# Kernel optimization log

Hardware: AMD Instinct MI355X
Metric: run time of the kernel (lower is better)

Reference implementation:

```python
import jax, jax.numpy as jnp
import numpy as np

N_HEAD = 16


def setup_inputs() -> dict:
    key = jax.random.key(0)
    ks = jax.random.split(key, 5)
    B, T, D_IN, D = 2, 2048, 1152, 1024
    s_in = 1.0 / np.sqrt(D_IN)
    s_d = 1.0 / np.sqrt(D)
    return {
        "xp": jax.random.normal(ks[0], (B, T, D_IN), jnp.float32),
        "Wq": jax.random.normal(ks[1], (D_IN, D), jnp.float32) * s_in,
        "bq": jnp.zeros((D,), jnp.float32),
        "Wk": jax.random.normal(ks[2], (D_IN, D), jnp.float32) * s_in,
        "bk": jnp.zeros((D,), jnp.float32),
        "Wv": jax.random.normal(ks[3], (D_IN, D), jnp.float32) * s_in,
        "bv": jnp.zeros((D,), jnp.float32),
        "Wp": jax.random.normal(ks[4], (D, D), jnp.float32) * s_d,
        "bp": jnp.zeros((D,), jnp.float32),
    }


def reference(xp, Wq, bq, Wk, bk, Wv, bv, Wp, bp):
    B, T, _ = xp.shape
    D = Wq.shape[1]
    hd = D // N_HEAD  # head dim
    # q, k, v projections -> [B, H, T, hd]
    def split_heads(t):
        return t.reshape(B, T, N_HEAD, hd).transpose(0, 2, 1, 3)
    q = split_heads(xp @ Wq + bq)
    k = split_heads(xp @ Wk + bk)
    v = split_heads(xp @ Wv + bv)
    scale = 1.0 / np.sqrt(hd).astype(np.float32)
    att = jnp.einsum("bhqd,bhkd->bhqk", q, k) * scale  # [B,H,T,T]
    causal = jnp.tril(jnp.ones((T, T), bool))
    att = jnp.where(causal[None, None], att, -jnp.inf)
    att = jax.nn.softmax(att, axis=-1)
    y = jnp.einsum("bhqk,bhkd->bhqd", att, v)  # [B,H,T,hd]
    y = y.transpose(0, 2, 1, 3).reshape(B, T, D)
    return y @ Wp + bp
```

## Files before the change

### kernel.cpp

```cpp
#include <hip/hip_runtime.h>
#include <hip/hip_bf16.h>

typedef __attribute__((ext_vector_type(8))) short bf16x8;
typedef __attribute__((ext_vector_type(4))) short bf16x4;
typedef __attribute__((ext_vector_type(4))) float f32x4;

__device__ __forceinline__ void gload_lds16(const void* g, void* l) {
    __builtin_amdgcn_global_load_lds(
        (const __attribute__((address_space(1))) unsigned int*)g,
        (__attribute__((address_space(3))) unsigned int*)l, 16, 0, 0);
}

__device__ __forceinline__ f32x4 mfma_16x16x16(bf16x4 a, bf16x4 b, f32x4 c) {
#if __has_builtin(__builtin_amdgcn_mfma_f32_16x16x16bf16_1k)
    return __builtin_amdgcn_mfma_f32_16x16x16bf16_1k(a, b, c, 0, 0, 0);
#else
    f32x4 d = c;
    asm volatile("v_mfma_f32_16x16x16_bf16 %0, %1, %2, %0" : "+v"(d) : "v"(a), "v"(b));
    return d;
#endif
}

__global__ void k_cvt_bf16(const float* __restrict__ x, __hip_bfloat16* __restrict__ o, int n8) {
    int i = blockIdx.x * 256 + threadIdx.x;
    if (i >= n8) return;
    const float4* xp = (const float4*)(x + (size_t)i * 8);
    float4 a = xp[0], b = xp[1];
    union { __hip_bfloat16 h[8]; uint4 u; } tu;
    tu.h[0] = __float2bfloat16(a.x); tu.h[1] = __float2bfloat16(a.y);
    tu.h[2] = __float2bfloat16(a.z); tu.h[3] = __float2bfloat16(a.w);
    tu.h[4] = __float2bfloat16(b.x); tu.h[5] = __float2bfloat16(b.y);
    tu.h[6] = __float2bfloat16(b.z); tu.h[7] = __float2bfloat16(b.w);
    *(uint4*)(o + (size_t)i * 8) = tu.u;
}

__global__ void k_tr3(const float* __restrict__ s0, const float* __restrict__ s1,
                      const float* __restrict__ s2, __hip_bfloat16* __restrict__ dst,
                      int K, int N) {
    __shared__ float tile[32][33];
    const float* src = (blockIdx.z == 0) ? s0 : ((blockIdx.z == 1) ? s1 : s2);
    __hip_bfloat16* d = dst + (size_t)blockIdx.z * N * K;
    int n0 = blockIdx.x * 32, k0 = blockIdx.y * 32;
    int tx = threadIdx.x & 31, ty = threadIdx.x >> 5;
#pragma unroll
    for (int i = 0; i < 4; i++)
        tile[ty + i * 8][tx] = src[(size_t)(k0 + ty + i * 8) * N + n0 + tx];
    __syncthreads();
#pragma unroll
    for (int i = 0; i < 4; i++)
        d[(size_t)(n0 + ty + i * 8) * K + k0 + tx] = __float2bfloat16(tile[tx][ty + i * 8]);
}

__global__ void k_tr(const float* __restrict__ src, __hip_bfloat16* __restrict__ dst, int K, int N) {
    __shared__ float tile[32][33];
    int n0 = blockIdx.x * 32, k0 = blockIdx.y * 32;
    int tx = threadIdx.x & 31, ty = threadIdx.x >> 5;
#pragma unroll
    for (int i = 0; i < 4; i++)
        tile[ty + i * 8][tx] = src[(size_t)(k0 + ty + i * 8) * N + n0 + tx];
    __syncthreads();
#pragma unroll
    for (int i = 0; i < 4; i++)
        dst[(size_t)(n0 + ty + i * 8) * K + k0 + tx] = __float2bfloat16(tile[tx][ty + i * 8]);
}

#define QSCALE 0.18033688011111204f

template <int EPI>
__global__ __launch_bounds__(256, 2) void k_gemm(
    const __hip_bfloat16* __restrict__ A, const __hip_bfloat16* __restrict__ Bt,
    int M, int N, int K,
    const float* __restrict__ b0, const float* __restrict__ b1, const float* __restrict__ b2,
    __hip_bfloat16* __restrict__ qb, __hip_bfloat16* __restrict__ kb, __hip_bfloat16* __restrict__ vb,
    float* __restrict__ outp, int mtiles)
{
    __shared__ __align__(16) __hip_bfloat16 As[128 * 64];
    __shared__ __align__(16) __hip_bfloat16 Bs[128 * 64];
    const int t = threadIdx.x;
    const int lane = t & 63, w = t >> 6;
    const int wr = w >> 1, wc = w & 1;
    const int r16 = lane & 15, kg = lane >> 4;
    const int cpx = gridDim.x >> 3;
    const int bid = blockIdx.x;
    const int swz = (bid & 7) * cpx + (bid >> 3);
    const int m0 = (swz % mtiles) * 128, n0 = (swz / mtiles) * 128;
    f32x4 acc[4][4] = {};
    const int ksteps = K >> 6;
    for (int kt = 0; kt < ksteps; ++kt) {
        if (kt) __syncthreads();
        const int ks = kt * 64;
#pragma unroll
        for (int i = 0; i < 4; i++) {
            int ci = i * 256 + t;
            int row = ci >> 3, kc = (ci & 7) * 8;
            gload_lds16(A + (size_t)(m0 + row) * K + ks + kc, As + ci * 8);
        }
#pragma unroll
        for (int i = 0; i < 4; i++) {
            int ci = i * 256 + t;
            int row = ci >> 3, kc = (ci & 7) * 8;
            gload_lds16(Bt + (size_t)(n0 + row) * K + ks + kc, Bs + ci * 8);
        }
        __syncthreads();
#pragma unroll
        for (int c = 0; c < 2; c++) {
            bf16x8 af[4], bfr[4];
#pragma unroll
            for (int mi = 0; mi < 4; mi++)
                af[mi] = *(const bf16x8*)(As + (wr * 64 + mi * 16 + r16) * 64 + c * 32 + kg * 8);
#pragma unroll
            for (int ni = 0; ni < 4; ni++)
                bfr[ni] = *(const bf16x8*)(Bs + (wc * 64 + ni * 16 + r16) * 64 + c * 32 + kg * 8);
#pragma unroll
            for (int mi = 0; mi < 4; mi++)
#pragma unroll
                for (int ni = 0; ni < 4; ni++)
                    acc[mi][ni] = __builtin_amdgcn_mfma_f32_16x16x32_bf16(af[mi], bfr[ni], acc[mi][ni], 0, 0, 0);
        }
    }
#pragma unroll
    for (int mi = 0; mi < 4; mi++) {
#pragma unroll
        for (int ni = 0; ni < 4; ni++) {
#pragma unroll
            for (int j = 0; j < 4; j++) {
                int m = m0 + wr * 64 + mi * 16 + kg * 4 + j;
                int n = n0 + wc * 64 + ni * 16 + r16;
                float val = acc[mi][ni][j];
                if (EPI == 0) {
                    int proj = n >> 10, r = n & 1023;
                    int hh = r >> 6, dd = r & 63;
                    int bb = m >> 11, tt = m & 2047;
                    if (proj == 0) {
                        val = (val + b0[r]) * QSCALE;
                        qb[((size_t)(bb * 16 + hh) * 2048 + tt) * 64 + dd] = __float2bfloat16(val);
                    } else if (proj == 1) {
                        val += b1[r];
                        kb[((size_t)(bb * 16 + hh) * 2048 + tt) * 64 + dd] = __float2bfloat16(val);
                    } else {
                        val += b2[r];
                        vb[((size_t)(bb * 16 + hh) * 64 + dd) * 2048 + tt] = __float2bfloat16(val);
                    }
                } else {
                    outp[(size_t)m * N + n] = val + b0[n];
                }
            }
        }
    }
}

__global__ __launch_bounds__(256, 4) void k_attn(
    const __hip_bfloat16* __restrict__ qbuf,
    const __hip_bfloat16* __restrict__ kbuf,
    const __hip_bfloat16* __restrict__ vtbuf,
    __hip_bfloat16* __restrict__ y)
{
    __shared__ __align__(16) __hip_bfloat16 Kl[2][64 * 64];
    __shared__ __align__(16) __hip_bfloat16 Vl[2][64 * 64];
    const int t = threadIdx.x, lane = t & 63, w = t >> 6;
    const int r16 = lane & 15, kg = lane >> 4;
    const int g = blockIdx.x;
    const int c4 = g >> 8, p = g & 255;
    const int bh = (p >> 5) * 4 + c4;
    const int rr = p & 31;
    const int qt = (c4 & 1) ? rr : 31 - rr;
    const int swr = (r16 & 7) << 3;
    const int q0 = qt * 64 + w * 16;
    const __hip_bfloat16* qp = qbuf + ((size_t)bh * 2048 + q0) * 64;
    bf16x8 qf0 = *(const bf16x8*)(qp + r16 * 64 + kg * 8);
    bf16x8 qf1 = *(const bf16x8*)(qp + r16 * 64 + 32 + kg * 8);
    f32x4 O[4] = {};
    float m_s = -3.0e38f, l_s = 0.f;
    const __hip_bfloat16* kb = kbuf + (size_t)bh * 2048 * 64;
    const __hip_bfloat16* vb = vtbuf + (size_t)bh * 64 * 2048;

    const int ci0 = t, ci1 = 256 + t;
    const int kr0 = ci0 >> 3, sc0 = ((ci0 & 7) * 8) ^ ((kr0 & 7) << 3);
    const int kr1 = ci1 >> 3, sc1 = ((ci1 & 7) * 8) ^ ((kr1 & 7) << 3);

    gload_lds16(kb + (size_t)kr0 * 64 + sc0, &Kl[0][ci0 * 8]);
    gload_lds16(kb + (size_t)kr1 * 64 + sc1, &Kl[0][ci1 * 8]);
    gload_lds16(vb + (size_t)kr0 * 2048 + sc0, &Vl[0][ci0 * 8]);
    gload_lds16(vb + (size_t)kr1 * 2048 + sc1, &Vl[0][ci1 * 8]);
    __syncthreads();

    for (int kt = 0; kt <= qt; ++kt) {
        const int cur = kt & 1;
        if (kt < qt) {
            const int kn = kt + 1;
            gload_lds16(kb + (size_t)kn * 4096 + (size_t)kr0 * 64 + sc0, &Kl[cur ^ 1][ci0 * 8]);
            gload_lds16(kb + (size_t)kn * 4096 + (size_t)kr1 * 64 + sc1, &Kl[cur ^ 1][ci1 * 8]);
            gload_lds16(vb + (size_t)kr0 * 2048 + kn * 64 + sc0, &Vl[cur ^ 1][ci0 * 8]);
            gload_lds16(vb + (size_t)kr1 * 2048 + kn * 64 + sc1, &Vl[cur ^ 1][ci1 * 8]);
        }
        const int kbase = kt * 64;
        if (kbase <= q0 + 15) {
            const __hip_bfloat16* Klb = Kl[cur];
            const __hip_bfloat16* Vlb = Vl[cur];
            f32x4 S[4];
            __builtin_amdgcn_s_setprio(1);
#pragma unroll
            for (int ct = 0; ct < 4; ct++) {
                f32x4 s = {};
                const int r = ct * 16 + r16;
                bf16x8 kf0 = *(const bf16x8*)(Klb + r * 64 + ((kg * 8) ^ swr));
                s = __builtin_amdgcn_mfma_f32_16x16x32_bf16(kf0, qf0, s, 0, 0, 0);
                bf16x8 kf1 = *(const bf16x8*)(Klb + r * 64 + ((32 + kg * 8) ^ swr));
                s = __builtin_amdgcn_mfma_f32_16x16x32_bf16(kf1, qf1, s, 0, 0, 0);
                S[ct] = s;
            }
            __builtin_amdgcn_s_setprio(0);
            if (kbase + 63 > q0) {
#pragma unroll
                for (int ct = 0; ct < 4; ct++)
#pragma unroll
                    for (int j = 0; j < 4; j++)
                        if (kbase + ct * 16 + kg * 4 + j > q0 + r16) S[ct][j] = -3.0e38f;
            }
            float rmax = S[0][0];
#pragma unroll
            for (int ct = 0; ct < 4; ct++)
#pragma unroll
                for (int j = 0; j < 4; j++) rmax = fmaxf(rmax, S[ct][j]);
            rmax = fmaxf(rmax, __shfl_xor(rmax, 16));
            rmax = fmaxf(rmax, __shfl_xor(rmax, 32));
            if (__any(rmax > m_s + 8.0f)) {
                const float mn = fmaxf(m_s, rmax);
                const float al = exp2f(m_s - mn);
                m_s = mn;
                l_s *= al;
#pragma unroll
                for (int j = 0; j < 4; j++) {
                    const float aj = __shfl(al, kg * 4 + j);
#pragma unroll
                    for (int ot = 0; ot < 4; ot++) O[ot][j] *= aj;
                }
            }
            float rsum = 0.f;
#pragma unroll
            for (int ct = 0; ct < 4; ct++)
#pragma unroll
                for (int j = 0; j < 4; j++) { S[ct][j] = exp2f(S[ct][j] - m_s); rsum += S[ct][j]; }
            rsum += __shfl_xor(rsum, 16);
            rsum += __shfl_xor(rsum, 32);
            l_s += rsum;
            bf16x4 pa[4];
#pragma unroll
            for (int ct = 0; ct < 4; ct++) {
                union { __hip_bfloat16 h[4]; bf16x4 v; } pk;
                pk.h[0] = __float2bfloat16(S[ct][0]);
                pk.h[1] = __float2bfloat16(S[ct][1]);
                pk.h[2] = __float2bfloat16(S[ct][2]);
                pk.h[3] = __float2bfloat16(S[ct][3]);
                pa[ct] = pk.v;
            }
            __builtin_amdgcn_s_setprio(1);
#pragma unroll
            for (int ot = 0; ot < 4; ot++) {
                const int vrow = ot * 16 + r16;
#pragma unroll
                for (int ct = 0; ct < 4; ct++) {
                    bf16x4 vf = *(const bf16x4*)(Vlb + vrow * 64 + ((ct * 16 + kg * 4) ^ ((vrow & 7) << 3)));
                    O[ot] = mfma_16x16x16(pa[ct], vf, O[ot]);
                }
            }
            __builtin_amdgcn_s_setprio(0);
        }
        __syncthreads();
    }
    const int b = bh >> 4, h = bh & 15;
    const float linv = 1.0f / l_s;
#pragma unroll
    for (int j = 0; j < 4; j++) {
        const float iv = __shfl(linv, kg * 4 + j);
        const int qq = q0 + kg * 4 + j;
#pragma unroll
        for (int ot = 0; ot < 4; ot++)
            y[((size_t)b * 2048 + qq) * 1024 + h * 64 + ot * 16 + r16] = __float2bfloat16(O[ot][j] * iv);
    }
}

extern "C" void kernel_launch(void* const* d_in, const int* in_sizes, int n_in,
                              void* d_out, int out_size, void* d_ws, size_t ws_size,
                              hipStream_t stream) {
    const float* xp = (const float*)d_in[0];
    const float* Wq = (const float*)d_in[1];
    const float* bq = (const float*)d_in[2];
    const float* Wk = (const float*)d_in[3];
    const float* bk = (const float*)d_in[4];
    const float* Wv = (const float*)d_in[5];
    const float* bv = (const float*)d_in[6];
    const float* Wp = (const float*)d_in[7];
    const float* bp = (const float*)d_in[8];
    float* out = (float*)d_out;

    char* ws = (char*)d_ws;
    __hip_bfloat16* xb     = (__hip_bfloat16*)(ws);
    __hip_bfloat16* Wqkv_t = (__hip_bfloat16*)(ws + 9437184);
    __hip_bfloat16* Wp_t   = (__hip_bfloat16*)(ws + 16515072);
    __hip_bfloat16* qb     = (__hip_bfloat16*)(ws + 18612224);
    __hip_bfloat16* kbv    = (__hip_bfloat16*)(ws + 27000832);
    __hip_bfloat16* vtb    = (__hip_bfloat16*)(ws + 35389440);
    __hip_bfloat16* yb     = (__hip_bfloat16*)(ws + 43778048);

    k_cvt_bf16<<<2304, 256, 0, stream>>>(xp, xb, 589824);
    dim3 trg3(1024 / 32, 1152 / 32, 3);
    k_tr3<<<trg3, 256, 0, stream>>>(Wq, Wk, Wv, Wqkv_t, 1152, 1024);
    dim3 trg2(1024 / 32, 1024 / 32);
    k_tr<<<trg2, 256, 0, stream>>>(Wp, Wp_t, 1024, 1024);

    k_gemm<0><<<768, 256, 0, stream>>>(xb, Wqkv_t, 4096, 3072, 1152, bq, bk, bv, qb, kbv, vtb,
                                       nullptr, 32);
    k_attn<<<1024, 256, 0, stream>>>(qb, kbv, vtb, yb);
    k_gemm<1><<<256, 256, 0, stream>>>(yb, Wp_t, 4096, 1024, 1024, bp, nullptr, nullptr,
                                       nullptr, nullptr, nullptr, out, 32);
}
```

Before: 157.2 us.

## Widen attention KV tile to 128 and use plain 2D GEMM grid

The attention kernel now stages 128 keys and values per iteration instead of 64, with 64 KB of double-buffered LDS, and processes eight score column tiles per step. This halves the number of loop iterations and barriers per block. In exchange it allows fewer resident blocks per CU (launch bound 4 to 2), raises register pressure, and does wasted masked work on the diagonal tile, which is now twice as wide. Separately, the GEMMs drop their XCD-aware block swizzle in favour of a plain 2D grid, which may change L2 locality.

Measured after the change: 159.1 us. About the same (+1.3%).

```diff
diff --git a/kernel.cpp b/kernel.cpp
--- a/kernel.cpp
+++ b/kernel.cpp
@@ -72,7 +72,7 @@
     int M, int N, int K,
     const float* __restrict__ b0, const float* __restrict__ b1, const float* __restrict__ b2,
     __hip_bfloat16* __restrict__ qb, __hip_bfloat16* __restrict__ kb, __hip_bfloat16* __restrict__ vb,
-    float* __restrict__ outp, int mtiles)
+    float* __restrict__ outp)
 {
     __shared__ __align__(16) __hip_bfloat16 As[128 * 64];
     __shared__ __align__(16) __hip_bfloat16 Bs[128 * 64];
@@ -80,10 +80,7 @@
     const int lane = t & 63, w = t >> 6;
     const int wr = w >> 1, wc = w & 1;
     const int r16 = lane & 15, kg = lane >> 4;
-    const int cpx = gridDim.x >> 3;
-    const int bid = blockIdx.x;
-    const int swz = (bid & 7) * cpx + (bid >> 3);
-    const int m0 = (swz % mtiles) * 128, n0 = (swz / mtiles) * 128;
+    const int m0 = blockIdx.x * 128, n0 = blockIdx.y * 128;
     f32x4 acc[4][4] = {};
     const int ksteps = K >> 6;
     for (int kt = 0; kt < ksteps; ++kt) {
@@ -149,14 +146,14 @@
     }
 }
 
-__global__ __launch_bounds__(256, 4) void k_attn(
+__global__ __launch_bounds__(256, 2) void k_attn(
     const __hip_bfloat16* __restrict__ qbuf,
     const __hip_bfloat16* __restrict__ kbuf,
     const __hip_bfloat16* __restrict__ vtbuf,
     __hip_bfloat16* __restrict__ y)
 {
-    __shared__ __align__(16) __hip_bfloat16 Kl[2][64 * 64];
-    __shared__ __align__(16) __hip_bfloat16 Vl[2][64 * 64];
+    __shared__ __align__(16) __hip_bfloat16 Kl[2][128 * 64];
+    __shared__ __align__(16) __hip_bfloat16 Vl[2][64 * 128];
     const int t = threadIdx.x, lane = t & 63, w = t >> 6;
     const int r16 = lane & 15, kg = lane >> 4;
     const int g = blockIdx.x;
@@ -164,6 +161,7 @@
     const int bh = (p >> 5) * 4 + c4;
     const int rr = p & 31;
     const int qt = (c4 & 1) ? rr : 31 - rr;
+    const int nt = (qt >> 1) + 1;
     const int swr = (r16 & 7) << 3;
     const int q0 = qt * 64 + w * 16;
     const __hip_bfloat16* qp = qbuf + ((size_t)bh * 2048 + q0) * 64;
@@ -174,33 +172,41 @@
     const __hip_bfloat16* kb = kbuf + (size_t)bh * 2048 * 64;
     const __hip_bfloat16* vb = vtbuf + (size_t)bh * 64 * 2048;
 
-    const int ci0 = t, ci1 = 256 + t;
-    const int kr0 = ci0 >> 3, sc0 = ((ci0 & 7) * 8) ^ ((kr0 & 7) << 3);
-    const int kr1 = ci1 >> 3, sc1 = ((ci1 & 7) * 8) ^ ((kr1 & 7) << 3);
-
-    gload_lds16(kb + (size_t)kr0 * 64 + sc0, &Kl[0][ci0 * 8]);
-    gload_lds16(kb + (size_t)kr1 * 64 + sc1, &Kl[0][ci1 * 8]);
-    gload_lds16(vb + (size_t)kr0 * 2048 + sc0, &Vl[0][ci0 * 8]);
-    gload_lds16(vb + (size_t)kr1 * 2048 + sc1, &Vl[0][ci1 * 8]);
+    int kroww[4], kcoll[4], vroww[4], vcoll[4];
+#pragma unroll
+    for (int c = 0; c < 4; c++) {
+        const int ci = c * 256 + t;
+        kroww[c] = ci >> 3; kcoll[c] = ((ci & 7) * 8) ^ ((kroww[c] & 7) << 3);
+        vroww[c] = ci >> 4; vcoll[c] = ((ci & 15) * 8) ^ ((vroww[c] & 7) << 3);
+    }
+
+    auto stage = [&](int buf, int kt) {
+#pragma unroll
+        for (int c = 0; c < 4; c++) {
+            const int ci = c * 256 + t;
+            gload_lds16(kb + ((size_t)kt * 128 + kroww[c]) * 64 + kcoll[c], &Kl[buf][ci * 8]);
+        }
+#pragma unroll
+        for (int c = 0; c < 4; c++) {
+            const int ci = c * 256 + t;
+            gload_lds16(vb + (size_t)vroww[c] * 2048 + kt * 128 + vcoll[c], &Vl[buf][ci * 8]);
+        }
+    };
+
+    stage(0, 0);
     __syncthreads();
 
-    for (int kt = 0; kt <= qt; ++kt) {
+    for (int kt = 0; kt < nt; ++kt) {
         const int cur = kt & 1;
-        if (kt < qt) {
-            const int kn = kt + 1;
-            gload_lds16(kb + (size_t)kn * 4096 + (size_t)kr0 * 64 + sc0, &Kl[cur ^ 1][ci0 * 8]);
-            gload_lds16(kb + (size_t)kn * 4096 + (size_t)kr1 * 64 + sc1, &Kl[cur ^ 1][ci1 * 8]);
-            gload_lds16(vb + (size_t)kr0 * 2048 + kn * 64 + sc0, &Vl[cur ^ 1][ci0 * 8]);
-            gload_lds16(vb + (size_t)kr1 * 2048 + kn * 64 + sc1, &Vl[cur ^ 1][ci1 * 8]);
-        }
-        const int kbase = kt * 64;
-        if (kbase <= q0 + 15) {
+        if (kt + 1 < nt) stage(cur ^ 1, kt + 1);
+        const int kbase = kt * 128;
+        {
             const __hip_bfloat16* Klb = Kl[cur];
             const __hip_bfloat16* Vlb = Vl[cur];
-            f32x4 S[4];
+            f32x4 S[8];
             __builtin_amdgcn_s_setprio(1);
 #pragma unroll
-            for (int ct = 0; ct < 4; ct++) {
+            for (int ct = 0; ct < 8; ct++) {
                 f32x4 s = {};
                 const int r = ct * 16 + r16;
                 bf16x8 kf0 = *(const bf16x8*)(Klb + r * 64 + ((kg * 8) ^ swr));
@@ -210,16 +216,16 @@
                 S[ct] = s;
             }
             __builtin_amdgcn_s_setprio(0);
-            if (kbase + 63 > q0) {
-#pragma unroll
-                for (int ct = 0; ct < 4; ct++)
+            if (kbase + 127 > q0) {
+#pragma unroll
+                for (int ct = 0; ct < 8; ct++)
 #pragma unroll
                     for (int j = 0; j < 4; j++)
                         if (kbase + ct * 16 + kg * 4 + j > q0 + r16) S[ct][j] = -3.0e38f;
             }
             float rmax = S[0][0];
 #pragma unroll
-            for (int ct = 0; ct < 4; ct++)
+            for (int ct = 0; ct < 8; ct++)
 #pragma unroll
                 for (int j = 0; j < 4; j++) rmax = fmaxf(rmax, S[ct][j]);
             rmax = fmaxf(rmax, __shfl_xor(rmax, 16));
@@ -238,15 +244,15 @@
             }
             float rsum = 0.f;
 #pragma unroll
-            for (int ct = 0; ct < 4; ct++)
+            for (int ct = 0; ct < 8; ct++)
 #pragma unroll
                 for (int j = 0; j < 4; j++) { S[ct][j] = exp2f(S[ct][j] - m_s); rsum += S[ct][j]; }
             rsum += __shfl_xor(rsum, 16);
             rsum += __shfl_xor(rsum, 32);
             l_s += rsum;
-            bf16x4 pa[4];
-#pragma unroll
-            for (int ct = 0; ct < 4; ct++) {
+            bf16x4 pa[8];
+#pragma unroll
+            for (int ct = 0; ct < 8; ct++) {
                 union { __hip_bfloat16 h[4]; bf16x4 v; } pk;
                 pk.h[0] = __float2bfloat16(S[ct][0]);
                 pk.h[1] = __float2bfloat16(S[ct][1]);
@@ -259,8 +265,8 @@
             for (int ot = 0; ot < 4; ot++) {
                 const int vrow = ot * 16 + r16;
 #pragma unroll
-                for (int ct = 0; ct < 4; ct++) {
-                    bf16x4 vf = *(const bf16x4*)(Vlb + vrow * 64 + ((ct * 16 + kg * 4) ^ ((vrow & 7) << 3)));
+                for (int ct = 0; ct < 8; ct++) {
+                    bf16x4 vf = *(const bf16x4*)(Vlb + vrow * 128 + ((ct * 16 + kg * 4) ^ swr));
                     O[ot] = mfma_16x16x16(pa[ct], vf, O[ot]);
                 }
             }
@@ -309,9 +315,10 @@
     dim3 trg2(1024 / 32, 1024 / 32);
     k_tr<<<trg2, 256, 0, stream>>>(Wp, Wp_t, 1024, 1024);
 
-    k_gemm<0><<<768, 256, 0, stream>>>(xb, Wqkv_t, 4096, 3072, 1152, bq, bk, bv, qb, kbv, vtb,
-                                       nullptr, 32);
+    dim3 g1(4096 / 128, 3072 / 128);
+    k_gemm<0><<<g1, 256, 0, stream>>>(xb, Wqkv_t, 4096, 3072, 1152, bq, bk, bv, qb, kbv, vtb, nullptr);
     k_attn<<<1024, 256, 0, stream>>>(qb, kbv, vtb, yb);
-    k_gemm<1><<<256, 256, 0, stream>>>(yb, Wp_t, 4096, 1024, 1024, bp, nullptr, nullptr,
-                                       nullptr, nullptr, nullptr, out, 32);
-}
+    dim3 g2(4096 / 128, 1024 / 128);
+    k_gemm<1><<<g2, 256, 0, stream>>>(yb, Wp_t, 4096, 1024, 1024, bp, nullptr, nullptr,
+                                      nullptr, nullptr, nullptr, out);
+}
```

## Stage V-projection tiles through LDS for coalesced transposed stores

Applied to the files above, without the earlier changes.

For the V third of the fused QKV GEMM, the epilogue now adds bias, packs to bf16, writes the tile transposed into XOR-swizzled shared memory, and then stores 16-byte vectors contiguous along time into the transposed V buffer. This replaces scattered 2-byte strided stores. The change also drops the blockIdx swizzle in favour of a plain 2D grid, which may reduce L2 locality. The price is extra LDS traffic and two barriers in the epilogue of V blocks.

Result: faster. 137.3 us (-12.7%).

```diff
diff --git a/kernel.cpp b/kernel.cpp
--- a/kernel.cpp
+++ b/kernel.cpp
@@ -4,11 +4,18 @@
 typedef __attribute__((ext_vector_type(8))) short bf16x8;
 typedef __attribute__((ext_vector_type(4))) short bf16x4;
 typedef __attribute__((ext_vector_type(4))) float f32x4;
+typedef __attribute__((ext_vector_type(2))) unsigned int u32x2;
 
 __device__ __forceinline__ void gload_lds16(const void* g, void* l) {
     __builtin_amdgcn_global_load_lds(
         (const __attribute__((address_space(1))) unsigned int*)g,
         (__attribute__((address_space(3))) unsigned int*)l, 16, 0, 0);
+}
+
+__device__ __forceinline__ unsigned int pk2(float x, float y) {
+    union { __hip_bfloat16 h[2]; unsigned int u; } z;
+    z.h[0] = __float2bfloat16(x); z.h[1] = __float2bfloat16(y);
+    return z.u;
 }
 
 __device__ __forceinline__ f32x4 mfma_16x16x16(bf16x4 a, bf16x4 b, f32x4 c) {
@@ -72,18 +79,16 @@
     int M, int N, int K,
     const float* __restrict__ b0, const float* __restrict__ b1, const float* __restrict__ b2,
     __hip_bfloat16* __restrict__ qb, __hip_bfloat16* __restrict__ kb, __hip_bfloat16* __restrict__ vb,
-    float* __restrict__ outp, int mtiles)
+    float* __restrict__ outp)
 {
-    __shared__ __align__(16) __hip_bfloat16 As[128 * 64];
-    __shared__ __align__(16) __hip_bfloat16 Bs[128 * 64];
+    __shared__ __align__(16) __hip_bfloat16 Sh[16384];
+    __hip_bfloat16* As = Sh;
+    __hip_bfloat16* Bs = Sh + 8192;
     const int t = threadIdx.x;
     const int lane = t & 63, w = t >> 6;
     const int wr = w >> 1, wc = w & 1;
     const int r16 = lane & 15, kg = lane >> 4;
-    const int cpx = gridDim.x >> 3;
-    const int bid = blockIdx.x;
-    const int swz = (bid & 7) * cpx + (bid >> 3);
-    const int m0 = (swz % mtiles) * 128, n0 = (swz / mtiles) * 128;
+    const int m0 = blockIdx.x * 128, n0 = blockIdx.y * 128;
     f32x4 acc[4][4] = {};
     const int ksteps = K >> 6;
     for (int kt = 0; kt < ksteps; ++kt) {
@@ -118,6 +123,37 @@
                     acc[mi][ni] = __builtin_amdgcn_mfma_f32_16x16x32_bf16(af[mi], bfr[ni], acc[mi][ni], 0, 0, 0);
         }
     }
+    if (EPI == 0 && n0 >= 2048) {
+        __syncthreads();
+#pragma unroll
+        for (int mi = 0; mi < 4; mi++) {
+#pragma unroll
+            for (int ni = 0; ni < 4; ni++) {
+                const int nl = wc * 64 + ni * 16 + r16;
+                const int mb = wr * 64 + mi * 16 + kg * 4;
+                const int r = n0 - 2048 + nl;
+                const float bias = b2[r];
+                u32x2 pk;
+                pk[0] = pk2(acc[mi][ni][0] + bias, acc[mi][ni][1] + bias);
+                pk[1] = pk2(acc[mi][ni][2] + bias, acc[mi][ni][3] + bias);
+                *(u32x2*)(Sh + nl * 128 + (mb ^ ((nl & 7) << 3))) = pk;
+            }
+        }
+        __syncthreads();
+#pragma unroll
+        for (int pass = 0; pass < 8; ++pass) {
+            const int ci = pass * 256 + t;
+            const int nl = ci >> 4;
+            const int ms = (ci & 15) * 8;
+            bf16x8 v = *(const bf16x8*)(Sh + nl * 128 + (ms ^ ((nl & 7) << 3)));
+            const int r = n0 - 2048 + nl;
+            const int hh = r >> 6, dd = r & 63;
+            const int m = m0 + ms;
+            const int bb = m >> 11, tt = m & 2047;
+            *(bf16x8*)(vb + ((size_t)(bb * 16 + hh) * 64 + dd) * 2048 + tt) = v;
+        }
+        return;
+    }
 #pragma unroll
     for (int mi = 0; mi < 4; mi++) {
 #pragma unroll
@@ -128,18 +164,15 @@
                 int n = n0 + wc * 64 + ni * 16 + r16;
                 float val = acc[mi][ni][j];
                 if (EPI == 0) {
-                    int proj = n >> 10, r = n & 1023;
+                    int r = n & 1023;
                     int hh = r >> 6, dd = r & 63;
                     int bb = m >> 11, tt = m & 2047;
-                    if (proj == 0) {
+                    if (n < 1024) {
                         val = (val + b0[r]) * QSCALE;
                         qb[((size_t)(bb * 16 + hh) * 2048 + tt) * 64 + dd] = __float2bfloat16(val);
-                    } else if (proj == 1) {
+                    } else {
                         val += b1[r];
                         kb[((size_t)(bb * 16 + hh) * 2048 + tt) * 64 + dd] = __float2bfloat16(val);
-                    } else {
-                        val += b2[r];
-                        vb[((size_t)(bb * 16 + hh) * 64 + dd) * 2048 + tt] = __float2bfloat16(val);
                     }
                 } else {
                     outp[(size_t)m * N + n] = val + b0[n];
@@ -309,9 +342,10 @@
     dim3 trg2(1024 / 32, 1024 / 32);
     k_tr<<<trg2, 256, 0, stream>>>(Wp, Wp_t, 1024, 1024);
 
-    k_gemm<0><<<768, 256, 0, stream>>>(xb, Wqkv_t, 4096, 3072, 1152, bq, bk, bv, qb, kbv, vtb,
-                                       nullptr, 32);
+    dim3 g1(4096 / 128, 3072 / 128);
+    k_gemm<0><<<g1, 256, 0, stream>>>(xb, Wqkv_t, 4096, 3072, 1152, bq, bk, bv, qb, kbv, vtb, nullptr);
     k_attn<<<1024, 256, 0, stream>>>(qb, kbv, vtb, yb);
-    k_gemm<1><<<256, 256, 0, stream>>>(yb, Wp_t, 4096, 1024, 1024, bp, nullptr, nullptr,
-                                       nullptr, nullptr, nullptr, out, 32);
-}
+    dim3 g2(4096 / 128, 1024 / 128);
+    k_gemm<1><<<g2, 256, 0, stream>>>(yb, Wp_t, 4096, 1024, 1024, bp, nullptr, nullptr,
+                                      nullptr, nullptr, nullptr, out);
+}
```
